# Kernel optimization log

Measured on AMD Instinct MI355X. Metric: run time of the kernel, lower is better.

Reference implementation:

```python
import jax, jax.numpy as jnp
import numpy as np

B, S, V, H = 16, 256, 32000, 1024
W_SCALE = 0.02


def setup_inputs() -> dict:
    key = jax.random.key(0)
    ks = jax.random.split(key, 8)
    inp = {
        "x": jax.random.randint(ks[0], (B, S), 0, V, dtype=jnp.int32),
        "emb": jax.random.normal(ks[1], (V, H), dtype=jnp.float32) * W_SCALE,
        "W_i": jax.random.normal(ks[2], (H, 2 * H), dtype=jnp.float32) * W_SCALE,
        "b_i": jnp.zeros((H,), dtype=jnp.float32),
        "W_f": jax.random.normal(ks[3], (H, 2 * H), dtype=jnp.float32) * W_SCALE,
        "b_f": jnp.ones((H,), dtype=jnp.float32),
        "W_o": jax.random.normal(ks[4], (H, 2 * H), dtype=jnp.float32) * W_SCALE,
        "b_o": jnp.zeros((H,), dtype=jnp.float32),
        "W_c": jax.random.normal(ks[5], (H, 2 * H), dtype=jnp.float32) * W_SCALE,
        "b_c": jnp.zeros((H,), dtype=jnp.float32),
        "fc_b": jnp.zeros((V,), dtype=jnp.float32),
    }
    return inp


def reference(x, emb, W_i, b_i, W_f, b_f, W_o, b_o, W_c, b_c, fc_b):
    # x: [B,S] int token ids. Embedding (tied with output proj), dropout is eval/no-op.
    xe = emb[x]                      # [B,S,H]
    xs = jnp.swapaxes(xe, 0, 1)      # [S,B,H] time-major, matches x.transpose(0,1)

    # Pack the 4 gate Linears into one [4H, 2H] GEMM per step (same math).
    W_all = jnp.concatenate([W_i, W_f, W_o, W_c], axis=0)   # [4H,2H]
    b_all = jnp.concatenate([b_i, b_f, b_o, b_c], axis=0)   # [4H]

    Hd = emb.shape[1]
    h0 = jnp.zeros((x.shape[0], Hd), dtype=emb.dtype)
    c0 = jnp.zeros((x.shape[0], Hd), dtype=emb.dtype)

    def step(carry, xt):
        h, c = carry
        hx = jnp.concatenate([h, xt], axis=1)                 # [B,2H]
        g = hx @ W_all.T + b_all                              # [B,4H]
        i, f, o, cc = jnp.split(g, 4, axis=1)
        c = jax.nn.sigmoid(f) * c + jax.nn.sigmoid(i) * jnp.tanh(cc)
        h = jax.nn.sigmoid(o) * jnp.tanh(c)
        return (h, c), h

    (h, c), ys = jax.lax.scan(step, (h0, c0), xs)             # ys: [S,B,H]
    # Tied output projection: fc.weight = embedding.weight
    logits = jnp.einsum('sbh,vh->sbv', ys, emb) + fc_b        # [S,B,V]
    logits = jnp.swapaxes(logits, 0, 1)                       # [B,S,V]
    return logits, h, c
```

## Files before the change

### kernel.cpp

```cpp
#include <hip/hip_runtime.h>
#include <hip/hip_bf16.h>

typedef __bf16 bf16;
typedef __bf16 bf16x8 __attribute__((ext_vector_type(8)));
typedef float  f32x4 __attribute__((ext_vector_type(4)));

#define B_  16
#define S_  256
#define V_  32000
#define H_  1024

static const size_t OFF_WH  = 65536000;
static const size_t OFF_WX  = OFF_WH  + 8388608;
static const size_t OFF_XE  = OFF_WX  + 8388608;
static const size_t OFF_YS  = OFF_XE  + 8388608;
static const size_t OFF_XCT = OFF_YS  + 8388608;
static const size_t OFF_CTR = OFF_XCT + 67108864;

__device__ __forceinline__ void frag_gather_f32(const float* __restrict__ row,
                                                int k_off, bf16* __restrict__ unit,
                                                int lane) {
  const float* p = row + k_off + ((lane >> 4) * 8);
  const float4 lo = *reinterpret_cast<const float4*>(p);
  const float4 hi = *reinterpret_cast<const float4*>(p + 4);
  bf16x8 v;
  v[0] = (bf16)lo.x; v[1] = (bf16)lo.y; v[2] = (bf16)lo.z; v[3] = (bf16)lo.w;
  v[4] = (bf16)hi.x; v[5] = (bf16)hi.y; v[6] = (bf16)hi.z; v[7] = (bf16)hi.w;
  *reinterpret_cast<bf16x8*>(unit + lane * 8) = v;
}

__global__ void k_init(unsigned* ctr) {
  if (threadIdx.x == 0) *ctr = 0u;
}

__global__ void k_convert_emb(const float* __restrict__ emb, bf16* __restrict__ emb_frag) {
  const int unit = blockIdx.x * 4 + (threadIdx.x >> 6);
  const int lane = threadIdx.x & 63;
  const int vt = unit >> 5;
  const int kc = unit & 31;
  const float* row = emb + (size_t)(vt * 16 + (lane & 15)) * H_;
  frag_gather_f32(row, kc * 32, emb_frag + (size_t)unit * 512, lane);
}

__global__ void k_convert_w(const float* __restrict__ Wi, const float* __restrict__ Wf,
                            const float* __restrict__ Wo, const float* __restrict__ Wc,
                            bf16* __restrict__ Wh_frag, bf16* __restrict__ Wx_frag) {
  const int unit = blockIdx.x * 4 + (threadIdx.x >> 6);
  const int lane = threadIdx.x & 63;
  const int which = unit >> 13;
  const int u  = unit & 8191;
  const int jt = u >> 5;
  const int kc = u & 31;
  const int j  = jt * 16 + (lane & 15);
  const int q  = j >> 10;
  const float* W = (q == 0) ? Wi : (q == 1) ? Wf : (q == 2) ? Wo : Wc;
  const float* row = W + (size_t)(j & 1023) * (2 * H_) + (which ? H_ : 0);
  bf16* dst = (which ? Wx_frag : Wh_frag) + (size_t)u * 512;
  frag_gather_f32(row, kc * 32, dst, lane);
}

__global__ void k_embed(const int* __restrict__ x, const float* __restrict__ emb,
                        bf16* __restrict__ xe_frag) {
  const int unit = blockIdx.x * 4 + (threadIdx.x >> 6);
  const int lane = threadIdx.x & 63;
  const int st = unit >> 5;
  const int kc = unit & 31;
  const int b  = lane & 15;
  const int tok = x[b * S_ + st];
  const float* row = emb + (size_t)tok * H_;
  frag_gather_f32(row, kc * 32, xe_frag + (size_t)unit * 512, lane);
}

__device__ __forceinline__ void gemm_main_128(const bf16* __restrict__ A_frag,
                                              const bf16* __restrict__ B_frag,
                                              int mtile, int ntile,
                                              bf16* smem, f32x4 acc[4][4]) {
  const int tid  = threadIdx.x;
  const int lane = tid & 63;
  const int w    = tid >> 6;
  const int wm   = w >> 1, wn = w & 1;
  bf16* Als = smem;
  bf16* Bls = smem + 8192;
  const f32x4 zero = {0.f, 0.f, 0.f, 0.f};
#pragma unroll
  for (int mi = 0; mi < 4; ++mi)
#pragma unroll
    for (int ni = 0; ni < 4; ++ni) acc[mi][ni] = zero;

  for (int it = 0; it < 16; ++it) {
    __syncthreads();
#pragma unroll
    for (int c0 = 0; c0 < 8; ++c0) {
      const int c   = w * 8 + c0;
      const int isB = c >> 4;
      const int ci  = c & 15;
      const int i   = ci >> 1;
      const int kc  = ci & 1;
      const bf16* gsrc =
          (isB ? B_frag + (size_t)((ntile * 8 + i) * 32 + it * 2 + kc) * 512
               : A_frag + (size_t)((mtile * 8 + i) * 32 + it * 2 + kc) * 512) +
          lane * 8;
      bf16* ldst = (isB ? Bls : Als) + (i * 2 + kc) * 512;
      __builtin_amdgcn_global_load_lds(
          (const __attribute__((address_space(1))) void*)gsrc,
          (__attribute__((address_space(3))) void*)ldst, 16, 0, 0);
    }
    __syncthreads();
#pragma unroll
    for (int kc = 0; kc < 2; ++kc) {
      bf16x8 af[4], bfv[4];
#pragma unroll
      for (int i = 0; i < 4; ++i)
        af[i] = *reinterpret_cast<const bf16x8*>(Als + ((wm * 4 + i) * 2 + kc) * 512 + lane * 8);
#pragma unroll
      for (int i = 0; i < 4; ++i)
        bfv[i] = *reinterpret_cast<const bf16x8*>(Bls + ((wn * 4 + i) * 2 + kc) * 512 + lane * 8);
#pragma unroll
      for (int mi = 0; mi < 4; ++mi)
#pragma unroll
        for (int ni = 0; ni < 4; ++ni)
          acc[mi][ni] = __builtin_amdgcn_mfma_f32_16x16x32_bf16(af[mi], bfv[ni], acc[mi][ni], 0, 0, 0);
    }
  }
}

__global__ __launch_bounds__(256) void k_xc(const bf16* __restrict__ xe_frag,
                                            const bf16* __restrict__ Wx_frag,
                                            const float* __restrict__ bi, const float* __restrict__ bfp,
                                            const float* __restrict__ bo, const float* __restrict__ bc,
                                            float* __restrict__ XcT) {
  __shared__ bf16 smem[16384];
  const int ntile = blockIdx.x, mtile = blockIdx.y;
  f32x4 acc[4][4];
  gemm_main_128(xe_frag, Wx_frag, mtile, ntile, smem, acc);
  const int tid = threadIdx.x, lane = tid & 63, w = tid >> 6;
  const int wm = w >> 1, wn = w & 1;
  const int q = (ntile * 128) >> 10;
  const float* bias = (q == 0) ? bi : (q == 1) ? bfp : (q == 2) ? bo : bc;
#pragma unroll
  for (int ni = 0; ni < 4; ++ni) {
    const int j = ntile * 128 + (wn * 4 + ni) * 16 + (lane & 15);
    const float bj = bias[j & 1023];
#pragma unroll
    for (int mi = 0; mi < 4; ++mi) {
      const int r0 = (mtile * 8 + wm * 4 + mi) * 16 + (lane >> 4) * 4;
      f32x4 v = acc[mi][ni];
      v[0] += bj; v[1] += bj; v[2] += bj; v[3] += bj;
      *reinterpret_cast<f32x4*>(XcT + (size_t)j * 4096 + r0) = v;
    }
  }
}

__global__ __launch_bounds__(256) void k_lstm(const bf16* __restrict__ Wh_frag,
                                              const float* __restrict__ XcT,
                                              bf16* __restrict__ ys_frag,
                                              float* __restrict__ out_hc,
                                              unsigned* __restrict__ ctr) {
  const int bid  = blockIdx.x;
  const int tid  = threadIdx.x;
  const int lane = tid & 63;
  const int w    = tid >> 6;
  __shared__ float gbuf[4][16][17];
  const int cb   = tid & 15;
  const int ccol = tid >> 4;
  float c_state = 0.f;
  const bf16* Wbase = Wh_frag + (size_t)(w * 64 + bid) * 32 * 512;

  for (int s = 0; s < S_; ++s) {
    f32x4 acc = {0.f, 0.f, 0.f, 0.f};
    if (s > 0) {
      const bf16* Abase = ys_frag + (size_t)(s - 1) * 32 * 512;
#pragma unroll 8
      for (int kc = 0; kc < 32; ++kc) {
        bf16x8 a  = *reinterpret_cast<const bf16x8*>(Abase + kc * 512 + lane * 8);
        bf16x8 bb = *reinterpret_cast<const bf16x8*>(Wbase + kc * 512 + lane * 8);
        acc = __builtin_amdgcn_mfma_f32_16x16x32_bf16(a, bb, acc, 0, 0, 0);
      }
    }
#pragma unroll
    for (int e = 0; e < 4; ++e)
      gbuf[w][(lane >> 4) * 4 + e][lane & 15] = acc[e];
    __syncthreads();

    const int jq = bid * 16 + ccol;
    const int r  = s * 16 + cb;
    const float g0 = gbuf[0][cb][ccol] + XcT[(size_t)(jq)        * 4096 + r];
    const float g1 = gbuf[1][cb][ccol] + XcT[(size_t)(1024 + jq) * 4096 + r];
    const float g2 = gbuf[2][cb][ccol] + XcT[(size_t)(2048 + jq) * 4096 + r];
    const float g3 = gbuf[3][cb][ccol] + XcT[(size_t)(3072 + jq) * 4096 + r];
    const float ig = 1.f / (1.f + __expf(-g0));
    const float fg = 1.f / (1.f + __expf(-g1));
    const float og = 1.f / (1.f + __expf(-g2));
    c_state = fg * c_state + ig * tanhf(g3);
    const float h = og * tanhf(c_state);

    const int chunk = jq >> 5;
    const int lp    = cb + 16 * ((jq >> 3) & 3);
    ys_frag[((size_t)s * 32 + chunk) * 512 + lp * 8 + (jq & 7)] = (bf16)h;
    if (s == S_ - 1) {
      out_hc[cb * H_ + jq]                = h;
      out_hc[B_ * H_ + cb * H_ + jq]      = c_state;
    }
    __syncthreads();
    if (s < S_ - 1) {
      if (tid == 0) {
        __hip_atomic_fetch_add(ctr, 1u, __ATOMIC_RELEASE, __HIP_MEMORY_SCOPE_AGENT);
        const unsigned target = 64u * (unsigned)(s + 1);
        while (__hip_atomic_load(ctr, __ATOMIC_RELAXED, __HIP_MEMORY_SCOPE_AGENT) < target)
          __builtin_amdgcn_s_sleep(2);
        (void)__hip_atomic_load(ctr, __ATOMIC_ACQUIRE, __HIP_MEMORY_SCOPE_AGENT);
      }
      __syncthreads();
    }
  }
}

__global__ __launch_bounds__(256) void k_proj(const bf16* __restrict__ ys_frag,
                                              const bf16* __restrict__ emb_frag,
                                              const float* __restrict__ fcb,
                                              float* __restrict__ out) {
  __shared__ bf16 smem[16384];
  const int ntile = blockIdx.x, mtile = blockIdx.y;
  f32x4 acc[4][4];
  gemm_main_128(ys_frag, emb_frag, mtile, ntile, smem, acc);
  const int tid = threadIdx.x, lane = tid & 63, w = tid >> 6;
  const int wm = w >> 1, wn = w & 1;
  const size_t bstride = (size_t)S_ * V_;
#pragma unroll
  for (int ni = 0; ni < 4; ++ni) {
    const int v = ntile * 128 + (wn * 4 + ni) * 16 + (lane & 15);
    const float bv = fcb[v];
#pragma unroll
    for (int mi = 0; mi < 4; ++mi) {
      const int s  = mtile * 8 + wm * 4 + mi;
      const int b0 = (lane >> 4) * 4;
      float* po = out + (size_t)b0 * bstride + (size_t)s * V_ + v;
#pragma unroll
      for (int e = 0; e < 4; ++e)
        po[(size_t)e * bstride] = acc[mi][ni][e] + bv;
    }
  }
}

extern "C" void kernel_launch(void* const* d_in, const int* in_sizes, int n_in,
                              void* d_out, int out_size, void* d_ws, size_t ws_size,
                              hipStream_t stream) {
  const int*   x   = (const int*)  d_in[0];
  const float* emb = (const float*)d_in[1];
  const float* Wi  = (const float*)d_in[2];
  const float* bi  = (const float*)d_in[3];
  const float* Wf  = (const float*)d_in[4];
  const float* bfp = (const float*)d_in[5];
  const float* Wo  = (const float*)d_in[6];
  const float* bo  = (const float*)d_in[7];
  const float* Wc  = (const float*)d_in[8];
  const float* bc  = (const float*)d_in[9];
  const float* fcb = (const float*)d_in[10];

  char* ws = (char*)d_ws;
  bf16*     emb_frag = (bf16*)ws;
  bf16*     Wh_frag  = (bf16*)(ws + OFF_WH);
  bf16*     Wx_frag  = (bf16*)(ws + OFF_WX);
  bf16*     xe_frag  = (bf16*)(ws + OFF_XE);
  bf16*     ys_frag  = (bf16*)(ws + OFF_YS);
  float*    XcT      = (float*)(ws + OFF_XCT);
  unsigned* ctr      = (unsigned*)(ws + OFF_CTR);

  float* out    = (float*)d_out;
  float* out_hc = out + (size_t)B_ * S_ * V_;

  k_init<<<1, 64, 0, stream>>>(ctr);
  k_convert_emb<<<16000, 256, 0, stream>>>(emb, emb_frag);
  k_convert_w<<<4096, 256, 0, stream>>>(Wi, Wf, Wo, Wc, Wh_frag, Wx_frag);
  k_embed<<<2048, 256, 0, stream>>>(x, emb, xe_frag);
  k_xc<<<dim3(32, 32), 256, 0, stream>>>(xe_frag, Wx_frag, bi, bfp, bo, bc, XcT);
  k_lstm<<<64, 256, 0, stream>>>(Wh_frag, XcT, ys_frag, out_hc, ctr);
  k_proj<<<dim3(250, 32), 256, 0, stream>>>(ys_frag, emb_frag, fcb, out);
}
```

Before: 2.993 ms.

## Restructure recurrent LSTM kernel: register-resident weights, LDS staging, per-block flag barrier

Result: faster. 2.443 ms (-18.4%).

```diff
diff --git a/kernel.cpp b/kernel.cpp
--- a/kernel.cpp
+++ b/kernel.cpp
@@ -15,7 +15,7 @@
 static const size_t OFF_XE  = OFF_WX  + 8388608;
 static const size_t OFF_YS  = OFF_XE  + 8388608;
 static const size_t OFF_XCT = OFF_YS  + 8388608;
-static const size_t OFF_CTR = OFF_XCT + 67108864;
+static const size_t OFF_FLG = OFF_XCT + 67108864;
 
 __device__ __forceinline__ void frag_gather_f32(const float* __restrict__ row,
                                                 int k_off, bf16* __restrict__ unit,
@@ -29,8 +29,8 @@
   *reinterpret_cast<bf16x8*>(unit + lane * 8) = v;
 }
 
-__global__ void k_init(unsigned* ctr) {
-  if (threadIdx.x == 0) *ctr = 0u;
+__global__ void k_init(unsigned* flags) {
+  flags[threadIdx.x] = 0u;
 }
 
 __global__ void k_convert_emb(const float* __restrict__ emb, bf16* __restrict__ emb_frag) {
@@ -155,60 +155,106 @@
                                               const float* __restrict__ XcT,
                                               bf16* __restrict__ ys_frag,
                                               float* __restrict__ out_hc,
-                                              unsigned* __restrict__ ctr) {
+                                              unsigned* __restrict__ flags) {
   const int bid  = blockIdx.x;
   const int tid  = threadIdx.x;
   const int lane = tid & 63;
   const int w    = tid >> 6;
+  __shared__ __align__(16) bf16 smemA[16384];
   __shared__ float gbuf[4][16][17];
+  __shared__ __align__(16) bf16 hstage[256];
   const int cb   = tid & 15;
   const int ccol = tid >> 4;
+  const int jq   = bid * 16 + ccol;
   float c_state = 0.f;
+
   const bf16* Wbase = Wh_frag + (size_t)(w * 64 + bid) * 32 * 512;
+  bf16x8 breg[32];
+#pragma unroll
+  for (int kc = 0; kc < 32; ++kc)
+    breg[kc] = *reinterpret_cast<const bf16x8*>(Wbase + kc * 512 + lane * 8);
+
+  float xc0 = XcT[(size_t)(jq)        * 4096 + cb];
+  float xc1 = XcT[(size_t)(1024 + jq) * 4096 + cb];
+  float xc2 = XcT[(size_t)(2048 + jq) * 4096 + cb];
+  float xc3 = XcT[(size_t)(3072 + jq) * 4096 + cb];
 
   for (int s = 0; s < S_; ++s) {
     f32x4 acc = {0.f, 0.f, 0.f, 0.f};
     if (s > 0) {
-      const bf16* Abase = ys_frag + (size_t)(s - 1) * 32 * 512;
-#pragma unroll 8
-      for (int kc = 0; kc < 32; ++kc) {
-        bf16x8 a  = *reinterpret_cast<const bf16x8*>(Abase + kc * 512 + lane * 8);
-        bf16x8 bb = *reinterpret_cast<const bf16x8*>(Wbase + kc * 512 + lane * 8);
-        acc = __builtin_amdgcn_mfma_f32_16x16x32_bf16(a, bb, acc, 0, 0, 0);
+      const bf16* Asrc = ys_frag + (size_t)(s - 1) * 16384;
+#pragma unroll
+      for (int r = 0; r < 8; ++r)
+        __builtin_amdgcn_global_load_lds(
+            (const __attribute__((address_space(1))) void*)(Asrc + r * 2048 + tid * 8),
+            (__attribute__((address_space(3))) void*)(smemA + r * 2048 + tid * 8),
+            16, 0, 0);
+      __syncthreads();
+      f32x4 p0 = {0.f,0.f,0.f,0.f}, p1 = p0, p2 = p0, p3 = p0;
+#pragma unroll
+      for (int kc = 0; kc < 32; kc += 4) {
+        bf16x8 a0 = *reinterpret_cast<const bf16x8*>(smemA + (kc + 0) * 512 + lane * 8);
+        bf16x8 a1 = *reinterpret_cast<const bf16x8*>(smemA + (kc + 1) * 512 + lane * 8);
+        bf16x8 a2 = *reinterpret_cast<const bf16x8*>(smemA + (kc + 2) * 512 + lane * 8);
+        bf16x8 a3 = *reinterpret_cast<const bf16x8*>(smemA + (kc + 3) * 512 + lane * 8);
+        p0 = __builtin_amdgcn_mfma_f32_16x16x32_bf16(a0, breg[kc + 0], p0, 0, 0, 0);
+        p1 = __builtin_amdgcn_mfma_f32_16x16x32_bf16(a1, breg[kc + 1], p1, 0, 0, 0);
+        p2 = __builtin_amdgcn_mfma_f32_16x16x32_bf16(a2, breg[kc + 2], p2, 0, 0, 0);
+        p3 = __builtin_amdgcn_mfma_f32_16x16x32_bf16(a3, breg[kc + 3], p3, 0, 0, 0);
       }
+      f32x4 t01 = p0 + p1, t23 = p2 + p3;
+      acc = t01 + t23;
     }
 #pragma unroll
     for (int e = 0; e < 4; ++e)
       gbuf[w][(lane >> 4) * 4 + e][lane & 15] = acc[e];
     __syncthreads();
 
-    const int jq = bid * 16 + ccol;
-    const int r  = s * 16 + cb;
-    const float g0 = gbuf[0][cb][ccol] + XcT[(size_t)(jq)        * 4096 + r];
-    const float g1 = gbuf[1][cb][ccol] + XcT[(size_t)(1024 + jq) * 4096 + r];
-    const float g2 = gbuf[2][cb][ccol] + XcT[(size_t)(2048 + jq) * 4096 + r];
-    const float g3 = gbuf[3][cb][ccol] + XcT[(size_t)(3072 + jq) * 4096 + r];
+    const float g0 = gbuf[0][cb][ccol] + xc0;
+    const float g1 = gbuf[1][cb][ccol] + xc1;
+    const float g2 = gbuf[2][cb][ccol] + xc2;
+    const float g3 = gbuf[3][cb][ccol] + xc3;
     const float ig = 1.f / (1.f + __expf(-g0));
     const float fg = 1.f / (1.f + __expf(-g1));
     const float og = 1.f / (1.f + __expf(-g2));
     c_state = fg * c_state + ig * tanhf(g3);
     const float h = og * tanhf(c_state);
 
-    const int chunk = jq >> 5;
-    const int lp    = cb + 16 * ((jq >> 3) & 3);
-    ys_frag[((size_t)s * 32 + chunk) * 512 + lp * 8 + (jq & 7)] = (bf16)h;
+    hstage[(cb + 16 * (ccol >> 3)) * 8 + (ccol & 7)] = (bf16)h;
     if (s == S_ - 1) {
-      out_hc[cb * H_ + jq]                = h;
-      out_hc[B_ * H_ + cb * H_ + jq]      = c_state;
+      out_hc[cb * H_ + jq]           = h;
+      out_hc[B_ * H_ + cb * H_ + jq] = c_state;
     }
     __syncthreads();
+
+    if (tid < 32)
+      *reinterpret_cast<bf16x8*>(ys_frag + ((size_t)s * 32 + (bid >> 1)) * 512 +
+                                 (bid & 1) * 256 + tid * 8) =
+          *reinterpret_cast<const bf16x8*>(hstage + tid * 8);
+
     if (s < S_ - 1) {
-      if (tid == 0) {
-        __hip_atomic_fetch_add(ctr, 1u, __ATOMIC_RELEASE, __HIP_MEMORY_SCOPE_AGENT);
-        const unsigned target = 64u * (unsigned)(s + 1);
-        while (__hip_atomic_load(ctr, __ATOMIC_RELAXED, __HIP_MEMORY_SCOPE_AGENT) < target)
-          __builtin_amdgcn_s_sleep(2);
-        (void)__hip_atomic_load(ctr, __ATOMIC_ACQUIRE, __HIP_MEMORY_SCOPE_AGENT);
+      if (tid == 0)
+        __hip_atomic_store(&flags[bid], (unsigned)(s + 1), __ATOMIC_RELEASE,
+                           __HIP_MEMORY_SCOPE_AGENT);
+      {
+        const int r = (s + 1) * 16 + cb;
+        xc0 = XcT[(size_t)(jq)        * 4096 + r];
+        xc1 = XcT[(size_t)(1024 + jq) * 4096 + r];
+        xc2 = XcT[(size_t)(2048 + jq) * 4096 + r];
+        xc3 = XcT[(size_t)(3072 + jq) * 4096 + r];
+      }
+      if (tid < 64) {
+        const unsigned target = (unsigned)(s + 1);
+        unsigned v = __hip_atomic_load(&flags[tid], __ATOMIC_RELAXED,
+                                       __HIP_MEMORY_SCOPE_AGENT);
+        while (!__all((int)(v >= target))) {
+          __builtin_amdgcn_s_sleep(1);
+          v = __hip_atomic_load(&flags[tid], __ATOMIC_RELAXED,
+                                __HIP_MEMORY_SCOPE_AGENT);
+        }
+        if (tid == 0)
+          (void)__hip_atomic_load(&flags[0], __ATOMIC_ACQUIRE,
+                                  __HIP_MEMORY_SCOPE_AGENT);
       }
       __syncthreads();
     }
@@ -264,16 +310,16 @@
   bf16*     xe_frag  = (bf16*)(ws + OFF_XE);
   bf16*     ys_frag  = (bf16*)(ws + OFF_YS);
   float*    XcT      = (float*)(ws + OFF_XCT);
-  unsigned* ctr      = (unsigned*)(ws + OFF_CTR);
+  unsigned* flags    = (unsigned*)(ws + OFF_FLG);
 
   float* out    = (float*)d_out;
   float* out_hc = out + (size_t)B_ * S_ * V_;
 
-  k_init<<<1, 64, 0, stream>>>(ctr);
+  k_init<<<1, 64, 0, stream>>>(flags);
   k_convert_emb<<<16000, 256, 0, stream>>>(emb, emb_frag);
   k_convert_w<<<4096, 256, 0, stream>>>(Wi, Wf, Wo, Wc, Wh_frag, Wx_frag);
   k_embed<<<2048, 256, 0, stream>>>(x, emb, xe_frag);
   k_xc<<<dim3(32, 32), 256, 0, stream>>>(xe_frag, Wx_frag, bi, bfp, bo, bc, XcT);
-  k_lstm<<<64, 256, 0, stream>>>(Wh_frag, XcT, ys_frag, out_hc, ctr);
+  k_lstm<<<64, 256, 0, stream>>>(Wh_frag, XcT, ys_frag, out_hc, flags);
   k_proj<<<dim3(250, 32), 256, 0, stream>>>(ys_frag, emb_frag, fcb, out);
 }
```
